# Performance work log

Measured on AMD Instinct MI355X. Metric: run time of the kernel, lower is better.

The kernel has to match this reference:

```python
import jax, jax.numpy as jnp
import numpy as np

SIZE = 5           # kernel size and num_rbfs
MUL = 16           # multiplicity of 0e and 1o in irreps_in/out
CROP = SIZE // 2
# e3nn FullyConnectedTensorProduct path weights (normalization='component', path_normalization='element'):
# path_weight = sqrt((2*l_out+1) / fan_in), fan_in = sum over paths into that output of mul1*mul2.
# out 0e: paths (0e,0e)+(1o,1o) -> fan_in=32; out 1o: paths (0e,1o)+(1o,0e) -> fan_in=32.
PW0 = (1.0 / 32.0) ** 0.5          # scalar output paths
PW1 = (3.0 / 32.0) ** 0.5          # vector output paths
INV_SQRT3 = 3.0 ** -0.5            # wigner-3j values: w3j(1,0,1)=w3j(0,1,1)=w3j(1,1,0)=delta/sqrt(3)


def _lattice_consts():
    # lattice of kernel offsets, steps=(1,1,1) keeps all SIZE points per axis
    r = jnp.linspace(-1.0, 1.0, SIZE)
    lat = jnp.stack(jnp.meshgrid(r, r, r, indexing='ij'), axis=-1)   # [5,5,5,3]
    d = jnp.linalg.norm(lat, axis=-1)                                # [5,5,5]
    # soft_one_hot_linspace(basis='smooth_finite', endpoint=True) over [0,1] with SIZE bins
    values = jnp.linspace(0.0, 1.0, SIZE)
    step = values[1] - values[0]
    diff = (d[..., None] - values) / step                            # [5,5,5,5]
    def sus(t):  # soft unit step: exp(-1/t) for t>0 else 0
        return jnp.where(t > 0, jnp.exp(-1.0 / jnp.where(t > 0, t, 1.0)), 0.0)
    emb = 1.14136 * np.float32(np.e ** 2) * sus(diff + 1.0) * sus(1.0 - diff)
    # spherical harmonics lmax=1, normalize=True, 'component' normalization
    n = lat / jnp.maximum(d, 1e-12)[..., None]                       # zero vector -> 0 (like F.normalize)
    sh0 = jnp.ones_like(d)                                           # l=0 component-normalized
    sh1 = (3.0 ** 0.5) * n                                           # l=1 component-normalized, [5,5,5,3]
    return emb, sh0, sh1


def _make_kernel(weight):
    """emb @ weight -> per-voxel TP weights; tp.right(sh, w) -> [5,5,5,in=64,out=64] kernel."""
    emb, sh0, sh1 = _lattice_consts()
    w = emb @ weight                                                 # [5,5,5,1024]
    S = w.shape[:3]
    blk = MUL * MUL
    # path order: (0e,0e->0e), (0e,1o->1o), (1o,0e->1o), (1o,1o->0e)
    w1, w2, w3, w4 = [w[..., i * blk:(i + 1) * blk].reshape(*S, MUL, MUL) for i in range(4)]
    k_ss = PW0 * w1 * sh0[..., None, None]                           # [s,u,w]   scalar in -> scalar out
    k_sv = PW1 * INV_SQRT3 * jnp.einsum('...uw,...k->...uwk', w2, sh1)   # [s,u,w,k] scalar in -> vector out
    k_vs = PW0 * INV_SQRT3 * jnp.einsum('...uw,...i->...uiw', w4, sh1)   # [s,u,i,w] vector in -> scalar out
    eye3 = jnp.eye(3, dtype=w.dtype)
    k_vv = PW1 * INV_SQRT3 * (w3 * sh0[..., None, None])[..., :, None, :, None] \
           * eye3[None, None, None, None, :, None, :]                # [s,u,i,w,k] vector in -> vector out
    top = jnp.concatenate([k_ss, k_sv.reshape(*S, MUL, 3 * MUL)], axis=-1)            # [s,16,64]
    bot = jnp.concatenate([k_vs.reshape(*S, 3 * MUL, MUL),
                           k_vv.reshape(*S, 3 * MUL, 3 * MUL)], axis=-1)              # [s,48,64]
    kernel = jnp.concatenate([top, bot], axis=-2)                    # [5,5,5,in,out]
    return jnp.transpose(kernel, (4, 3, 0, 1, 2))                    # 'xyzio->oixyz'


def reference(x, weight, w_sc0, w_sc1):
    B = x.shape[0]
    sp = x.shape[2:]
    # self-connection: e3nn Linear (per-irrep mixing, 1/sqrt(fan_in) norm), then crop
    xs = x[:, :MUL]                                                  # scalars [B,16,X,Y,Z]
    xv = x[:, MUL:].reshape(B, MUL, 3, *sp)                          # vectors [B,16,3,X,Y,Z]
    inv = 1.0 / MUL ** 0.5
    sc_s = jnp.einsum('buxyz,uw->bwxyz', xs, w_sc0) * inv
    sc_v = (jnp.einsum('buixyz,uw->bwixyz', xv, w_sc1) * inv).reshape(B, 3 * MUL, *sp)
    sc = jnp.concatenate([sc_s, sc_v], axis=1)[:, :, CROP:-CROP, CROP:-CROP, CROP:-CROP]
    # equivariant kernel + dense conv3d (torch conv3d = correlation = VALID conv here)
    kernel = _make_kernel(weight)                                    # [64,64,5,5,5]
    conv = jax.lax.conv_general_dilated(x, kernel, (1, 1, 1), 'VALID',
                                        dimension_numbers=('NCDHW', 'OIDHW', 'NCDHW'))
    return sc + conv


def setup_inputs() -> dict:
    key = jax.random.key(0)
    k1, k2, k3, k4 = jax.random.split(key, 4)
    weight_numel = 4 * MUL * MUL  # 1024
    return {
        'x': jax.random.normal(k1, (1, 4 * MUL, 56, 56, 56), dtype=jnp.float32),
        'weight': jax.random.normal(k2, (SIZE, weight_numel), dtype=jnp.float32)
                  * np.float32((2.0 / weight_numel) ** 0.5),  # kaiming_normal(relu)
        'w_sc0': jax.random.normal(k3, (MUL, MUL), dtype=jnp.float32),
        'w_sc1': jax.random.normal(k4, (MUL, MUL), dtype=jnp.float32),
    }
```

## Files before the change

kernel.cpp:

```cpp
#include <hip/hip_runtime.h>
#include <hip/hip_bf16.h>

typedef unsigned short ush;
typedef __bf16 v8bf __attribute__((ext_vector_type(8)));
typedef float f32x4 __attribute__((ext_vector_type(4)));
typedef float f32x16 __attribute__((ext_vector_type(16)));

#define SPD 56
#define OSD 52
#define SP3 175616
#define NCX 5488
#define NBA 2112
#define N_A_ELEMS (264*2048)

__global__ void aux_kernel(const float* __restrict__ x, ush* __restrict__ xb,
                           const float* __restrict__ weight, const float* __restrict__ w_sc0,
                           const float* __restrict__ w_sc1, ush* __restrict__ A) {
    __shared__ float t[64 * 33];
    const int bid = blockIdx.x;
    const int tid = threadIdx.x;
    if (bid < NCX) {
        const int s0 = (bid % 2744) * 64;
        const int cg = bid / 2744;
        const int w = tid >> 6, l = tid & 63;
        #pragma unroll
        for (int k = 0; k < 8; k++) {
            int c = w * 8 + k;
            t[l * 33 + c] = x[(cg * 32 + c) * SP3 + s0 + l];
        }
        __syncthreads();
        int v = tid >> 2, qq = tid & 3;
        union { ush u[8]; uint4 q4; } pk;
        #pragma unroll
        for (int j = 0; j < 8; j++) {
            __hip_bfloat16 b = __float2bfloat16(t[v * 33 + qq * 8 + j]);
            pk.u[j] = *(ush*)&b;
        }
        *(uint4*)(xb + ((size_t)(cg * SP3 + s0 + v)) * 32 + qq * 8) = pk.q4;
        return;
    }
    int f = (bid - NCX) * 256 + tid;
    if (f >= N_A_ELEMS) return;
    int c   = f & 31;
    int o   = (f >> 5) & 63;
    int T   = f >> 11;
    int cg  = (T >= 128) ? 1 : 0;
    int tau = T - cg * 128;
    if (tau >= 125) { A[f] = 0; return; }
    int i   = cg * 32 + c;
    int dz = tau / 25, dy = (tau / 5) % 5, dx = tau % 5;
    float rz = -1.f + 0.5f * dz, ry = -1.f + 0.5f * dy, rx = -1.f + 0.5f * dx;
    float d = sqrtf(rz * rz + ry * ry + rx * rx);
    float dm = fmaxf(d, 1e-12f);
    float nv[3] = { rz / dm, ry / dm, rx / dm };
    float emb[5];
    #pragma unroll
    for (int m = 0; m < 5; m++) {
        float diff = 4.f * d - (float)m;
        float ta = diff + 1.f, tb = 1.f - diff;
        float sa = ta > 0.f ? expf(-1.f / ta) : 0.f;
        float sb = tb > 0.f ? expf(-1.f / tb) : 0.f;
        emb[m] = 1.14136f * 7.3890560989306495f * sa * sb;
    }
    const float PW0 = 0.17677669529663687f;
    const float PW1 = 0.30618621784789724f;
    const float IS3 = 0.57735026918962576f;
    float val = 0.f;
    int widx = -1; float scale = 0.f;
    if (i < 16) {
        if (o < 16) { widx = i * 16 + o;                         scale = PW0; }
        else        { int wc = (o - 16) / 3, kc = (o - 16) % 3;
                      widx = 256 + i * 16 + wc;                  scale = PW1 * nv[kc]; }
    } else {
        int u = (i - 16) / 3, ic = (i - 16) % 3;
        if (o < 16) { widx = 768 + u * 16 + o;                   scale = PW0 * nv[ic]; }
        else        { int wc = (o - 16) / 3, jc = (o - 16) % 3;
                      if (ic == jc) { widx = 512 + u * 16 + wc;  scale = PW1 * IS3; } }
    }
    if (widx >= 0) {
        float wv = 0.f;
        #pragma unroll
        for (int m = 0; m < 5; m++) wv += emb[m] * weight[m * 1024 + widx];
        val = scale * wv;
    }
    if (tau == 62) {
        if (i < 16 && o < 16) val += 0.25f * w_sc0[i * 16 + o];
        else if (i >= 16 && o >= 16) {
            int u = (i - 16) / 3, ic = (i - 16) % 3;
            int wc = (o - 16) / 3, jc = (o - 16) % 3;
            if (ic == jc) val += 0.25f * w_sc1[u * 16 + wc];
        }
    }
    __hip_bfloat16 b = __float2bfloat16(val);
    A[f] = *(ush*)&b;
}

__launch_bounds__(256, 2)
__global__ void conv_main(const ush* __restrict__ A, const ush* __restrict__ xb,
                          float* __restrict__ out) {
    __shared__ ush patch[32768];

    const int b  = blockIdx.x;
    const int bp = (b & 7) * 148 + (b >> 3);
    if (bp >= 1183) return;
    const int bx = bp % 13;
    const int t1 = bp / 13;
    const int by = t1 % 13;
    const int bz = t1 / 13;
    const int x0 = bx * 4, y0 = by * 4;
    const int z0 = (bz == 6) ? 44 : bz * 8;

    const int tid  = threadIdx.x;
    const int wv   = tid >> 6;
    const int lane = tid & 63;
    const int lhi  = lane >> 5;
    const int rbase32 = ((lane >> 4) & 1) * 64 + ((lane >> 2) & 3) * 8 + (lane & 3);
    const int t0 = wv * 32;

    f32x16 acc[2][4];
    #pragma unroll
    for (int mt = 0; mt < 2; mt++)
        #pragma unroll
        for (int nt = 0; nt < 4; nt++)
            acc[mt][nt] = (f32x16)(0.f);

    int dz, dy, dx;
    v8bf afA[2][2], afB[2][2];
    v8bf b0A[4], b0B[4], b1A[4], b1B[4];

    auto SLOTS = [&](int& s0, int& s1) {
        int vb = dz * 64 + dy * 8 + dx;
        if (vb > 292) vb = 0;
        int v0 = vb + rbase32;
        int pre = v0 + (v0 >> 3);
        s0 = v0 * 4 + ((lhi + pre) & 3);
        s1 = v0 * 4 + ((2 + lhi + pre) & 3);
    };
    auto ADV = [&]() {
        int c1 = (dx == 4);
        dx = c1 ? 0 : dx + 1;
        int c2 = c1 & (dy == 4);
        dy = c2 ? 0 : dy + c1;
        dz += c2;
    };
    auto LDB = [&](v8bf (&bf)[4], int slot) {
        #pragma unroll
        for (int nt = 0; nt < 4; nt++)
            bf[nt] = *(const v8bf*)(patch + slot * 8 + nt * 4096);
    };
    auto LDA = [&](v8bf (&af)[2][2], const ush* p) {
        #pragma unroll
        for (int mt = 0; mt < 2; mt++)
            #pragma unroll
            for (int h = 0; h < 2; h++)
                af[mt][h] = *(const v8bf*)(p + mt * 1024 + h * 16);
    };
    auto MM0 = [&](v8bf (&af)[2][2], v8bf (&bf)[4]) {
        #pragma unroll
        for (int mt = 0; mt < 2; mt++)
            #pragma unroll
            for (int nt = 0; nt < 4; nt++)
                acc[mt][nt] = __builtin_amdgcn_mfma_f32_32x32x16_bf16(af[mt][0], bf[nt], acc[mt][nt], 0, 0, 0);
    };
    auto MM1 = [&](v8bf (&af)[2][2], v8bf (&bf)[4]) {
        #pragma unroll
        for (int mt = 0; mt < 2; mt++)
            #pragma unroll
            for (int nt = 0; nt < 4; nt++)
                acc[mt][nt] = __builtin_amdgcn_mfma_f32_32x32x16_bf16(af[mt][1], bf[nt], acc[mt][nt], 0, 0, 0);
    };

    for (int cg = 0; cg < 2; cg++) {
        const ush* Ap = A + ((size_t)(cg * 128 + t0)) * 2048 + (lane & 31) * 32 + lhi * 8;
        LDA(afA, Ap);

        __syncthreads();
        #pragma unroll 4
        for (int it = 0; it < 12; it++) {
            int u   = tid + it * 256;
            int qq  = u & 3;
            int vox = u >> 2;
            int xp = vox & 7, yp = (vox >> 3) & 7, zp = vox >> 6;
            const ush* g = xb + ((size_t)((cg * SPD + z0 + zp) * SPD + (y0 + yp)) * SPD + (x0 + xp)) * 32 + qq * 8;
            uint4 v = *(const uint4*)g;
            int slot = vox * 4 + ((qq + vox + (vox >> 3)) & 3);
            *(uint4*)(patch + slot * 8) = v;
        }
        __syncthreads();

        dz = t0 / 25; int rr = t0 - dz * 25; dy = rr / 5; dx = rr - dy * 5;
        int s0, s1;
        SLOTS(s0, s1);
        LDB(b0A, s0);
        LDB(b1A, s1);
        ADV();

        #pragma unroll 1
        for (int j = 0; j < 32; j += 2) {
            SLOTS(s0, s1);
            LDB(b0B, s0);
            LDA(afB, Ap + 2048);
            MM0(afA, b0A);
            LDB(b1B, s1);
            MM1(afA, b1A);
            ADV(); Ap += 2048;
            SLOTS(s0, s1);
            LDB(b0A, s0);
            LDA(afA, Ap + 2048);
            MM0(afB, b0B);
            LDB(b1A, s1);
            MM1(afB, b1B);
            ADV(); Ap += 2048;
        }
    }

    __syncthreads();
    float* red = (float*)patch;
    if (wv >= 2) {
        #pragma unroll
        for (int mt = 0; mt < 2; mt++)
            #pragma unroll
            for (int nt = 0; nt < 4; nt++) {
                float* p = red + (wv - 2) * 8192 + (mt * 4 + nt) * 1024 + lane * 16;
                #pragma unroll
                for (int s = 0; s < 4; s++) {
                    f32x4 v = { acc[mt][nt][s*4+0], acc[mt][nt][s*4+1], acc[mt][nt][s*4+2], acc[mt][nt][s*4+3] };
                    *(f32x4*)(p + s * 4) = v;
                }
            }
    }
    __syncthreads();
    if (wv < 2) {
        #pragma unroll
        for (int mt = 0; mt < 2; mt++)
            #pragma unroll
            for (int nt = 0; nt < 4; nt++) {
                float* p = red + wv * 8192 + (mt * 4 + nt) * 1024 + lane * 16;
                #pragma unroll
                for (int s = 0; s < 4; s++) {
                    f32x4 v = *(const f32x4*)(p + s * 4);
                    f32x4 m = { acc[mt][nt][s*4+0], acc[mt][nt][s*4+1], acc[mt][nt][s*4+2], acc[mt][nt][s*4+3] };
                    *(f32x4*)(p + s * 4) = v + m;
                }
            }
    }
    __syncthreads();

    const int yy = y0 + ((lane >> 2) & 3);
    const int xx = x0 + (lane & 3);
    #pragma unroll
    for (int k = 0; k < 2; k++) {
        int fi = wv * 2 + k;
        int mt = fi >> 2, nt = fi & 3;
        int zz = z0 + nt * 2 + ((lane >> 4) & 1);
        #pragma unroll
        for (int s = 0; s < 4; s++) {
            f32x4 v = *(const f32x4*)(red + fi * 1024 + lane * 16 + s * 4);
            v += *(const f32x4*)(red + 8192 + fi * 1024 + lane * 16 + s * 4);
            #pragma unroll
            for (int e = 0; e < 4; e++) {
                int o = mt * 32 + e + 8 * s + 4 * lhi;
                out[((o * OSD + zz) * OSD + yy) * OSD + xx] = v[e];
            }
        }
    }
}

extern "C" void kernel_launch(void* const* d_in, const int* in_sizes, int n_in,
                              void* d_out, int out_size, void* d_ws, size_t ws_size,
                              hipStream_t stream) {
    const float* x      = (const float*)d_in[0];
    const float* weight = (const float*)d_in[1];
    const float* w_sc0  = (const float*)d_in[2];
    const float* w_sc1  = (const float*)d_in[3];
    float* out = (float*)d_out;

    ush* A  = (ush*)d_ws;
    ush* xb = (ush*)((char*)d_ws + (2 << 20));

    aux_kernel<<<NCX + NBA, 256, 0, stream>>>(x, xb, weight, w_sc0, w_sc1, A);
    conv_main<<<1184, 256, 0, stream>>>(A, xb, out);
}
```

Before: 231.4 us.

## Skip kernel taps whose radial embedding is identically zero

Kernel taps with two or more coordinates on the lattice edge lie at distance at least sqrt(2). The smooth-finite radial basis is exactly zero there, so their weights are always zero. This change compacts the weight matrix A to the 81 active taps, padded to 88 so each of the four waves handles 22. It also builds a small lookup table of patch offsets per tap, which the conv loop reads instead of stepping dz/dy/dx. This cuts the MFMA and LDS work of the main conv by roughly a third, at the cost of an extra table read in the inner loop and a serial tap search in the aux kernel.

```diff
diff --git a/kernel.cpp b/kernel.cpp
--- a/kernel.cpp
+++ b/kernel.cpp
@@ -10,12 +10,22 @@
 #define OSD 52
 #define SP3 175616
 #define NCX 5488
-#define NBA 2112
-#define N_A_ELEMS (264*2048)
+#define NTAP 88
+#define NROW 177
+#define N_A_ELEMS (NROW*2048)
+#define NBA (N_A_ELEMS/256)
+#define VBT_OFF 393216
+
+__device__ __forceinline__ int tap_active(int tau) {
+    int dz = tau / 25, dy = (tau / 5) % 5, dx = tau % 5;
+    int e = (dz == 0 || dz == 4) + (dy == 0 || dy == 4) + (dx == 0 || dx == 4);
+    return e < 2;
+}
 
 __global__ void aux_kernel(const float* __restrict__ x, ush* __restrict__ xb,
                            const float* __restrict__ weight, const float* __restrict__ w_sc0,
-                           const float* __restrict__ w_sc1, ush* __restrict__ A) {
+                           const float* __restrict__ w_sc1, ush* __restrict__ A,
+                           ush* __restrict__ vbt) {
     __shared__ float t[64 * 33];
     const int bid = blockIdx.x;
     const int tid = threadIdx.x;
@@ -39,14 +49,34 @@
         *(uint4*)(xb + ((size_t)(cg * SP3 + s0 + v)) * 32 + qq * 8) = pk.q4;
         return;
     }
+    if (bid == NCX && tid < 90) {
+        int vb = 0;
+        if (tid < 81) {
+            int cnt = 0;
+            for (int tt = 0; tt < 125; tt++) {
+                if (tap_active(tt)) {
+                    if (cnt == tid) { vb = (tt / 25) * 64 + ((tt / 5) % 5) * 8 + (tt % 5); break; }
+                    cnt++;
+                }
+            }
+        }
+        vbt[tid] = (ush)vb;
+    }
     int f = (bid - NCX) * 256 + tid;
     if (f >= N_A_ELEMS) return;
-    int c   = f & 31;
-    int o   = (f >> 5) & 63;
-    int T   = f >> 11;
-    int cg  = (T >= 128) ? 1 : 0;
-    int tau = T - cg * 128;
-    if (tau >= 125) { A[f] = 0; return; }
+    int c    = f & 31;
+    int o    = (f >> 5) & 63;
+    int T    = f >> 11;
+    int cg   = (T >= NTAP) ? 1 : 0;
+    int tidx = T - cg * NTAP;
+    if (tidx >= 81) { A[f] = 0; return; }
+    int tau = 0, cnt = 0;
+    for (int tt = 0; tt < 125; tt++) {
+        if (tap_active(tt)) {
+            if (cnt == tidx) { tau = tt; break; }
+            cnt++;
+        }
+    }
     int i   = cg * 32 + c;
     int dz = tau / 25, dy = (tau / 5) % 5, dx = tau % 5;
     float rz = -1.f + 0.5f * dz, ry = -1.f + 0.5f * dy, rx = -1.f + 0.5f * dx;
@@ -96,8 +126,8 @@
 }
 
 __launch_bounds__(256, 2)
-__global__ void conv_main(const ush* __restrict__ A, const ush* __restrict__ xb,
-                          float* __restrict__ out) {
+__global__ void conv_main(const ush* __restrict__ A, const ush* __restrict__ vbt,
+                          const ush* __restrict__ xb, float* __restrict__ out) {
     __shared__ ush patch[32768];
 
     const int b  = blockIdx.x;
@@ -115,7 +145,7 @@
     const int lane = tid & 63;
     const int lhi  = lane >> 5;
     const int rbase32 = ((lane >> 4) & 1) * 64 + ((lane >> 2) & 3) * 8 + (lane & 3);
-    const int t0 = wv * 32;
+    const int t0 = wv * 22;
 
     f32x16 acc[2][4];
     #pragma unroll
@@ -124,25 +154,15 @@
         for (int nt = 0; nt < 4; nt++)
             acc[mt][nt] = (f32x16)(0.f);
 
-    int dz, dy, dx;
     v8bf afA[2][2], afB[2][2];
     v8bf b0A[4], b0B[4], b1A[4], b1B[4];
 
-    auto SLOTS = [&](int& s0, int& s1) {
-        int vb = dz * 64 + dy * 8 + dx;
-        if (vb > 292) vb = 0;
+    auto SLOTS = [&](int vb, int& s0, int& s1) {
         int v0 = vb + rbase32;
         int pre = v0 + (v0 >> 3);
         s0 = v0 * 4 + ((lhi + pre) & 3);
         s1 = v0 * 4 + ((2 + lhi + pre) & 3);
     };
-    auto ADV = [&]() {
-        int c1 = (dx == 4);
-        dx = c1 ? 0 : dx + 1;
-        int c2 = c1 & (dy == 4);
-        dy = c2 ? 0 : dy + c1;
-        dz += c2;
-    };
     auto LDB = [&](v8bf (&bf)[4], int slot) {
         #pragma unroll
         for (int nt = 0; nt < 4; nt++)
@@ -171,8 +191,10 @@
     };
 
     for (int cg = 0; cg < 2; cg++) {
-        const ush* Ap = A + ((size_t)(cg * 128 + t0)) * 2048 + (lane & 31) * 32 + lhi * 8;
+        const ush* Ap = A + ((size_t)(cg * NTAP + t0)) * 2048 + (lane & 31) * 32 + lhi * 8;
         LDA(afA, Ap);
+        int vb0 = vbt[t0];
+        int vbn = vbt[t0 + 1];
 
         __syncthreads();
         #pragma unroll 4
@@ -188,29 +210,29 @@
         }
         __syncthreads();
 
-        dz = t0 / 25; int rr = t0 - dz * 25; dy = rr / 5; dx = rr - dy * 5;
         int s0, s1;
-        SLOTS(s0, s1);
+        SLOTS(vb0, s0, s1);
         LDB(b0A, s0);
         LDB(b1A, s1);
-        ADV();
 
         #pragma unroll 1
-        for (int j = 0; j < 32; j += 2) {
-            SLOTS(s0, s1);
+        for (int j = 0; j < 22; j += 2) {
+            SLOTS(vbn, s0, s1);
             LDB(b0B, s0);
             LDA(afB, Ap + 2048);
             MM0(afA, b0A);
             LDB(b1B, s1);
             MM1(afA, b1A);
-            ADV(); Ap += 2048;
-            SLOTS(s0, s1);
+            vbn = vbt[t0 + j + 2];
+            Ap += 2048;
+            SLOTS(vbn, s0, s1);
             LDB(b0A, s0);
             LDA(afA, Ap + 2048);
             MM0(afB, b0B);
             LDB(b1A, s1);
             MM1(afB, b1B);
-            ADV(); Ap += 2048;
+            vbn = vbt[t0 + j + 3];
+            Ap += 2048;
         }
     }
 
@@ -275,9 +297,10 @@
     const float* w_sc1  = (const float*)d_in[3];
     float* out = (float*)d_out;
 
-    ush* A  = (ush*)d_ws;
-    ush* xb = (ush*)((char*)d_ws + (2 << 20));
-
-    aux_kernel<<<NCX + NBA, 256, 0, stream>>>(x, xb, weight, w_sc0, w_sc1, A);
-    conv_main<<<1184, 256, 0, stream>>>(A, xb, out);
+    ush* A   = (ush*)d_ws;
+    ush* vbt = A + VBT_OFF;
+    ush* xb  = (ush*)((char*)d_ws + (2 << 20));
+
+    aux_kernel<<<NCX + NBA, 256, 0, stream>>>(x, xb, weight, w_sc0, w_sc1, A, vbt);
+    conv_main<<<1184, 256, 0, stream>>>(A, vbt, xb, out);
 }
```

Measured after the change: 215.9 us. 6.7% less time.
